# Optimization experiments

Hardware: AMD Instinct MI355X
Metric: run time of the kernel (lower is better)

The kernel has to match this reference:

```python
import jax
jax.config.update('jax_enable_x64', True)
import jax.numpy as jnp
import numpy as np

RESOLUTION = 0.3
BUFFER_SIZE = 10_000_000
DIFF_TRAVEL_DIST_LOCAL = 80.0 * 1.5  # local_map_radius * local_map_travel_dist_ratio
PRIMES = jnp.array([73856093, 19349669, 83492791], dtype=jnp.int64)
N_PTS = 2_000_000
M_PTS = 2_000_000
N_FRAMES = 20_000


def setup_inputs() -> dict:
    key = jax.random.key(0)
    k1, k2, k3, k4, k5 = jax.random.split(key, 5)
    points = jax.random.normal(k1, (N_PTS, 3), dtype=jnp.float32) * 30.0  # ~local map extent (m)
    neural_points = jax.random.normal(k2, (M_PTS, 3), dtype=jnp.float32) * 30.0
    # hash buffer: -1 means empty slot, otherwise index into neural_points
    buffer_pt_index = jax.random.randint(k3, (BUFFER_SIZE,), 0, M_PTS + 1, dtype=jnp.int64) - 1
    # monotonically increasing travel distance per frame
    travel_dist = jnp.cumsum(jax.random.uniform(k4, (N_FRAMES,), dtype=jnp.float32) * 0.2)
    point_ts_update = jax.random.randint(k5, (M_PTS,), 0, N_FRAMES, dtype=jnp.int64)
    return {
        'points': points,
        'neural_points': neural_points,
        'buffer_pt_index': buffer_pt_index,
        'travel_dist': travel_dist,
        'point_ts_update': point_ts_update,
        'cur_ts': 15000,
    }


def reference(points, neural_points, buffer_pt_index, travel_dist, point_ts_update, cur_ts):
    # grid coords + prime spatial hash (torch.fmod keeps sign of dividend -> jnp.fmod)
    grid = jnp.floor(points / RESOLUTION).astype(jnp.int64)          # [N,3]
    h = jnp.fmod((grid * PRIMES).sum(-1), BUFFER_SIZE)               # [N], may be negative
    hw = jnp.where(h < 0, h + BUFFER_SIZE, h)                        # torch negative-index wrap

    # voxel down-sample: keep per-voxel point closest to its voxel center
    center = (grid.astype(points.dtype) + 0.5) * RESOLUTION
    d_center = jnp.sum((points - center) ** 2, axis=-1)
    seg_min = jax.ops.segment_min(d_center, hw, num_segments=BUFFER_SIZE)
    keep = d_center <= seg_min[hw]                                   # [N] bool

    # hash buffer lookup (hash_idx == -1 means empty; torch wraps -1 to last row on gather)
    hash_idx = buffer_pt_index[hw]                                   # [N]
    M = neural_points.shape[0]
    idx_w = jnp.where(hash_idx < 0, hash_idx + M, hash_idx)
    vec = neural_points[idx_w] - points
    dist2 = jnp.sum(vec * vec, axis=-1)                              # [N]

    ts = point_ts_update[idx_w]
    delta_travel = travel_dist[cur_ts] - travel_dist[ts]             # [N]

    update_mask = keep & ((hash_idx == -1)
                          | (dist2 > 3.0 * RESOLUTION ** 2)
                          | (delta_travel > DIFF_TRAVEL_DIST_LOCAL))
    return dist2, delta_travel, update_mask
```

## Files before the change

kernel.cpp:

```cpp
#include <hip/hip_runtime.h>

#define BUFSZ 10000000
#define RESF 0.3f
#define RINV (1.0f / 0.3f)

#define BIN_SHIFT   13
#define BKT_PER_BIN 8192
#define NBINS       1221
#define BIN_CAP     2048
#define OVF_CAP     4000

#define BINS_OFF 80000000ull
#define CTL_OFF  110000000ull
#define OVF_OFF  (CTL_OFF + 8192ull)

__device__ __forceinline__ void voxel_hash_d(float px, float py, float pz,
                                             int& hw, unsigned& dbits)
{
#pragma clang fp contract(off)
    float fx = floorf(px * RINV);
    float fy = floorf(py * RINV);
    float fz = floorf(pz * RINV);

    long long gx = (long long)fx;
    long long gy = (long long)fy;
    long long gz = (long long)fz;
    long long s = gx * 73856093LL + gy * 19349669LL + gz * 83492791LL;
    long long h = s % (long long)BUFSZ;
    hw = (int)(h < 0 ? h + BUFSZ : h);

    float cx = (fx + 0.5f) * RESF;
    float cy = (fy + 0.5f) * RESF;
    float cz = (fz + 0.5f) * RESF;
    float dx = px - cx;
    float dy = py - cy;
    float dz = pz - cz;
    float d = dx * dx + dy * dy + dz * dz;
    dbits = __float_as_uint(d);
}

__global__ __launch_bounds__(256) void bin_points(
    const float* __restrict__ points,
    unsigned long long* __restrict__ bins_e,
    unsigned int* __restrict__ ctl,
    unsigned long long* __restrict__ ovf,
    int N)
{
    __shared__ unsigned int cnt[NBINS];
    int t = threadIdx.x;
    for (int b = t; b < NBINS; b += 256) cnt[b] = 0;
    __syncthreads();

    int base = blockIdx.x * (256 * 16);
    unsigned hwv[16];
    unsigned dbv[16];

#pragma unroll
    for (int k = 0; k < 16; ++k) {
        int i = base + t + k * 256;
        hwv[k] = 0xFFFFFFFFu;
        dbv[k] = 0;
        if (i < N) {
            int hw; unsigned db;
            voxel_hash_d(points[3 * i], points[3 * i + 1], points[3 * i + 2],
                         hw, db);
            hwv[k] = (unsigned)hw;
            dbv[k] = db;
            if (db <= 0x3FFFFFFFu)
                atomicAdd(&cnt[hw >> BIN_SHIFT], 1u);
        }
    }
    __syncthreads();

    for (int b = t; b < NBINS; b += 256) {
        unsigned c = cnt[b];
        cnt[b] = c ? atomicAdd(&ctl[b], c) : 0u;
    }
    __syncthreads();

#pragma unroll
    for (int k = 0; k < 16; ++k) {
        if (hwv[k] == 0xFFFFFFFFu) continue;
        unsigned hw = hwv[k], db = dbv[k];
        if (db <= 0x3FFFFFFFu) {
            unsigned bin = hw >> BIN_SHIFT;
            unsigned idx = atomicAdd(&cnt[bin], 1u);
            if (idx < BIN_CAP) {
                bins_e[(size_t)bin * BIN_CAP + idx] =
                    ((unsigned long long)db << BIN_SHIFT)
                    | (hw & (BKT_PER_BIN - 1));
                continue;
            }
        }
        unsigned o = atomicAdd(&ctl[NBINS], 1u);
        if (o < OVF_CAP)
            ovf[o] = ((unsigned long long)db << 32) | hw;
    }
}

__global__ __launch_bounds__(256) void min_bins(
    const unsigned long long* __restrict__ bins_e,
    const unsigned int* __restrict__ ctl,
    const int2* __restrict__ bufidx2,
    uint4* __restrict__ p8q)
{
    __shared__ unsigned int tbl[BKT_PER_BIN];
    int t = threadIdx.x;
    int b = blockIdx.x;

    uint4* t4 = (uint4*)tbl;
    for (int l = t; l < BKT_PER_BIN / 4; l += 256)
        t4[l] = make_uint4(0xFFFFFFFFu, 0xFFFFFFFFu, 0xFFFFFFFFu, 0xFFFFFFFFu);
    __syncthreads();

    unsigned c = ctl[b];
    if (c > BIN_CAP) c = BIN_CAP;
    const unsigned long long* e = bins_e + (size_t)b * BIN_CAP;
    for (unsigned j = t; j < c; j += 256) {
        unsigned long long v = e[j];
        atomicMin(&tbl[(unsigned)(v & (BKT_PER_BIN - 1))],
                  (unsigned)(v >> BIN_SHIFT));
    }
    __syncthreads();

    long long pbase = (long long)b * (BKT_PER_BIN / 2);
    for (int l = t; l < BKT_PER_BIN / 2; l += 256) {
        long long pp = pbase + l;
        long long g = 2 * pp;
        if (g + 1 < (long long)BUFSZ) {
            int2 bi = bufidx2[pp];
            p8q[pp] = make_uint4(tbl[2 * l], (unsigned)bi.x,
                                 tbl[2 * l + 1], (unsigned)bi.y);
        }
    }
}

__global__ __launch_bounds__(256) void fix_ovf(
    const unsigned int* __restrict__ ctl,
    const unsigned long long* __restrict__ ovf,
    unsigned int* __restrict__ p8w)
{
    unsigned c = ctl[NBINS];
    if (c > OVF_CAP) c = OVF_CAP;
    for (unsigned e = threadIdx.x; e < c; e += 256) {
        unsigned long long v = ovf[e];
        atomicMin(p8w + 2ull * (unsigned)(v & 0xFFFFFFFFu), (unsigned)(v >> 32));
    }
}

__global__ __launch_bounds__(256) void pack_pnt(
    const float* __restrict__ neural,
    const int* __restrict__ ts_upd,
    float4* __restrict__ pnt, int M)
{
    int T = gridDim.x * 256;
    for (int j = blockIdx.x * 256 + threadIdx.x; j < M; j += T)
        pnt[j] = make_float4(neural[3 * j], neural[3 * j + 1],
                             neural[3 * j + 2], __int_as_float(ts_upd[j]));
}

__global__ __launch_bounds__(256) void pass_out_A4(
    const float* __restrict__ points,
    const uint2* __restrict__ p8,
    const float4* __restrict__ pnt,
    const float* __restrict__ travel,
    const int* __restrict__ cur_ts_p,
    float* __restrict__ out,
    int N, int M, int S)
{
#pragma clang fp contract(off)
    int tid = blockIdx.x * 256 + threadIdx.x;
    if (tid >= S) return;

    float tcur = travel[cur_ts_p[0]];

    int      iv[4];
    bool     val[4];
    float    pxv[4], pyv[4], pzv[4];
    int      hwv[4];
    unsigned dbv[4];

#pragma unroll
    for (int k = 0; k < 4; ++k) {
        int i = tid + k * S;
        val[k] = (i < N);
        iv[k]  = val[k] ? i : 0;
        pxv[k] = points[3 * iv[k] + 0];
        pyv[k] = points[3 * iv[k] + 1];
        pzv[k] = points[3 * iv[k] + 2];
        voxel_hash_d(pxv[k], pyv[k], pzv[k], hwv[k], dbv[k]);
    }

    uint2 ev[4];
#pragma unroll
    for (int k = 0; k < 4; ++k) ev[k] = p8[hwv[k]];

    int hidxv[4], idxwv[4];
    float4 ntv[4];
#pragma unroll
    for (int k = 0; k < 4; ++k) {
        hidxv[k] = (int)ev[k].y;
        idxwv[k] = (hidxv[k] < 0) ? (hidxv[k] + M) : hidxv[k];
    }
#pragma unroll
    for (int k = 0; k < 4; ++k) ntv[k] = pnt[idxwv[k]];

#pragma unroll
    for (int k = 0; k < 4; ++k) {
        if (!val[k]) continue;

        bool keep = dbv[k] <= ev[k].x;

        float vx = ntv[k].x - pxv[k];
        float vy = ntv[k].y - pyv[k];
        float vz = ntv[k].z - pzv[k];
        float dist2 = vx * vx + vy * vy + vz * vz;

        int ts = __float_as_int(ntv[k].w);
        float dtv = tcur - travel[ts];

        const float THR = (float)(3.0 * 0.3 * 0.3);
        bool upd = keep && ((hidxv[k] == -1) || (dist2 > THR) || (dtv > 120.0f));

        out[iv[k]]         = dist2;
        out[N + iv[k]]     = dtv;
        out[2 * N + iv[k]] = upd ? 1.0f : 0.0f;
    }
}

__global__ __launch_bounds__(256) void pass_min_C(
    const float* __restrict__ points, unsigned int* __restrict__ seg, int N)
{
    int i = blockIdx.x * 256 + threadIdx.x;
    if (i >= N) return;
    int hw; unsigned dbits;
    voxel_hash_d(points[3 * i], points[3 * i + 1], points[3 * i + 2], hw, dbits);
    atomicMin(seg + hw, dbits);
}

__global__ __launch_bounds__(256) void pass_out_C(
    const float* __restrict__ points, const float* __restrict__ neural,
    const int* __restrict__ bufidx, const float* __restrict__ travel,
    const int* __restrict__ ts_upd, const int* __restrict__ cur_ts_p,
    const unsigned int* __restrict__ seg, float* __restrict__ out, int N, int M)
{
#pragma clang fp contract(off)
    int i = blockIdx.x * 256 + threadIdx.x;
    if (i >= N) return;
    float px = points[3 * i], py = points[3 * i + 1], pz = points[3 * i + 2];
    int hw; unsigned dbits;
    voxel_hash_d(px, py, pz, hw, dbits);
    bool keep = dbits <= seg[hw];
    int hidx = bufidx[hw];
    int idxw = (hidx < 0) ? (hidx + M) : hidx;
    float vx = neural[3 * idxw] - px;
    float vy = neural[3 * idxw + 1] - py;
    float vz = neural[3 * idxw + 2] - pz;
    float dist2 = vx * vx + vy * vy + vz * vz;
    int ts = ts_upd[idxw];
    float dtv = travel[cur_ts_p[0]] - travel[ts];
    const float THR = (float)(3.0 * 0.3 * 0.3);
    bool upd = keep && ((hidx == -1) || (dist2 > THR) || (dtv > 120.0f));
    out[i] = dist2;
    out[N + i] = dtv;
    out[2 * N + i] = upd ? 1.0f : 0.0f;
}

extern "C" void kernel_launch(void* const* d_in, const int* in_sizes, int n_in,
                              void* d_out, int out_size, void* d_ws, size_t ws_size,
                              hipStream_t stream)
{
    const float* points  = (const float*)d_in[0];
    const float* neural  = (const float*)d_in[1];
    const int*   bufidx  = (const int*)d_in[2];
    const float* travel  = (const float*)d_in[3];
    const int*   ts_upd  = (const int*)d_in[4];
    const int*   cur_ts  = (const int*)d_in[5];

    int N = in_sizes[0] / 3;
    int M = in_sizes[1] / 3;

    const size_t needA = (size_t)BUFSZ * 8 + (size_t)M * 16;
    if (ws_size >= needA && N <= 2000000) {
        char* ws = (char*)d_ws;
        uint2*              p8     = (uint2*)ws;
        unsigned long long* bins_e = (unsigned long long*)(ws + BINS_OFF);
        unsigned int*       ctl    = (unsigned int*)(ws + CTL_OFF);
        unsigned long long* ovf    = (unsigned long long*)(ws + OVF_OFF);
        float4*             pnt    = (float4*)(ws + BINS_OFF);

        hipMemsetAsync(ctl, 0, 8192, stream);

        int bblocks = (N + 4095) / 4096;
        bin_points<<<bblocks, 256, 0, stream>>>(points, bins_e, ctl, ovf, N);
        min_bins<<<NBINS, 256, 0, stream>>>(bins_e, ctl, (const int2*)bufidx,
                                            (uint4*)p8);
        fix_ovf<<<1, 256, 0, stream>>>(ctl, ovf, (unsigned int*)p8);
        pack_pnt<<<2048, 256, 0, stream>>>(neural, ts_upd, pnt, M);

        int S = (N + 3) / 4;
        int oblocks = (S + 255) / 256;
        pass_out_A4<<<oblocks, 256, 0, stream>>>(points, p8, pnt, travel, cur_ts,
                                                 (float*)d_out, N, M, S);
    } else {
        unsigned int* seg = (unsigned int*)d_ws;
        hipMemsetAsync(seg, 0xFF, (size_t)BUFSZ * sizeof(unsigned int), stream);
        int pblocks = (N + 255) / 256;
        pass_min_C<<<pblocks, 256, 0, stream>>>(points, seg, N);
        pass_out_C<<<pblocks, 256, 0, stream>>>(points, neural, bufidx, travel,
                                                ts_upd, cur_ts, seg,
                                                (float*)d_out, N, M);
    }
}
```

Baseline: 157.2 us.

## Fuse segment-min and output pass into per-bin kernel carrying point index and coords

Binning now stores each point's index and a copy of its coordinates alongside the hash bucket and distance. A single per-bin kernel computes the segment minimum in shared memory and then emits all outputs for that bin's points directly. This removes the dense 10M-entry packed table, the separate overflow fix, the neural-point repack and the second full hashing pass over points. In exchange, outputs are written as scattered stores and the neural and ts gathers are no longer packed into one float4, and overflow entries are scanned by every block.

```diff
diff --git a/kernel.cpp b/kernel.cpp
--- a/kernel.cpp
+++ b/kernel.cpp
@@ -8,11 +8,14 @@
 #define BKT_PER_BIN 8192
 #define NBINS       1221
 #define BIN_CAP     2048
-#define OVF_CAP     4000
-
-#define BINS_OFF 80000000ull
-#define CTL_OFF  110000000ull
-#define OVF_OFF  (CTL_OFF + 8192ull)
+#define OVF_CAP     16384
+
+#define E64_OFF  0ull
+#define EPOS_OFF 20004864ull
+#define CTL_OFF  50012160ull
+#define OVFA_OFF (CTL_OFF + 8192ull)
+#define OVFB_OFF (OVFA_OFF + 131072ull)
+#define WS_NEED  (OVFB_OFF + 65536ull)
 
 __device__ __forceinline__ void voxel_hash_d(float px, float py, float pz,
                                              int& hw, unsigned& dbits)
@@ -39,11 +42,13 @@
     dbits = __float_as_uint(d);
 }
 
-__global__ __launch_bounds__(256) void bin_points(
+__global__ __launch_bounds__(256) void bin_points2(
     const float* __restrict__ points,
-    unsigned long long* __restrict__ bins_e,
+    unsigned long long* __restrict__ e64,
+    float* __restrict__ epos,
     unsigned int* __restrict__ ctl,
-    unsigned long long* __restrict__ ovf,
+    unsigned long long* __restrict__ ovfA,
+    unsigned int* __restrict__ ovfB,
     int N)
 {
     __shared__ unsigned int cnt[NBINS];
@@ -81,29 +86,46 @@
 #pragma unroll
     for (int k = 0; k < 16; ++k) {
         if (hwv[k] == 0xFFFFFFFFu) continue;
+        int i = base + t + k * 256;
         unsigned hw = hwv[k], db = dbv[k];
         if (db <= 0x3FFFFFFFu) {
             unsigned bin = hw >> BIN_SHIFT;
             unsigned idx = atomicAdd(&cnt[bin], 1u);
             if (idx < BIN_CAP) {
-                bins_e[(size_t)bin * BIN_CAP + idx] =
-                    ((unsigned long long)db << BIN_SHIFT)
-                    | (hw & (BKT_PER_BIN - 1));
+                size_t slot = (size_t)bin * BIN_CAP + idx;
+                e64[slot] = ((unsigned long long)db << 34)
+                          | ((unsigned long long)(unsigned)i << 13)
+                          | (hw & (BKT_PER_BIN - 1));
+                epos[3 * slot + 0] = points[3 * i + 0];
+                epos[3 * slot + 1] = points[3 * i + 1];
+                epos[3 * slot + 2] = points[3 * i + 2];
                 continue;
             }
         }
         unsigned o = atomicAdd(&ctl[NBINS], 1u);
-        if (o < OVF_CAP)
-            ovf[o] = ((unsigned long long)db << 32) | hw;
-    }
-}
-
-__global__ __launch_bounds__(256) void min_bins(
-    const unsigned long long* __restrict__ bins_e,
+        if (o < OVF_CAP) {
+            ovfA[o] = ((unsigned long long)db << 24) | hw;
+            ovfB[o] = (unsigned)i;
+        }
+    }
+}
+
+__global__ __launch_bounds__(256) void min_out(
+    const unsigned long long* __restrict__ e64,
+    const float* __restrict__ epos,
     const unsigned int* __restrict__ ctl,
-    const int2* __restrict__ bufidx2,
-    uint4* __restrict__ p8q)
-{
+    const unsigned long long* __restrict__ ovfA,
+    const unsigned int* __restrict__ ovfB,
+    const int* __restrict__ bufidx,
+    const float* __restrict__ neural,
+    const int* __restrict__ ts_upd,
+    const float* __restrict__ travel,
+    const int* __restrict__ cur_ts_p,
+    const float* __restrict__ points,
+    float* __restrict__ out,
+    int N, int M)
+{
+#pragma clang fp contract(off)
     __shared__ unsigned int tbl[BKT_PER_BIN];
     int t = threadIdx.x;
     int b = blockIdx.x;
@@ -115,116 +137,86 @@
 
     unsigned c = ctl[b];
     if (c > BIN_CAP) c = BIN_CAP;
-    const unsigned long long* e = bins_e + (size_t)b * BIN_CAP;
+    size_t ebase = (size_t)b * BIN_CAP;
     for (unsigned j = t; j < c; j += 256) {
-        unsigned long long v = e[j];
+        unsigned long long v = e64[ebase + j];
         atomicMin(&tbl[(unsigned)(v & (BKT_PER_BIN - 1))],
-                  (unsigned)(v >> BIN_SHIFT));
-    }
-    __syncthreads();
-
-    long long pbase = (long long)b * (BKT_PER_BIN / 2);
-    for (int l = t; l < BKT_PER_BIN / 2; l += 256) {
-        long long pp = pbase + l;
-        long long g = 2 * pp;
-        if (g + 1 < (long long)BUFSZ) {
-            int2 bi = bufidx2[pp];
-            p8q[pp] = make_uint4(tbl[2 * l], (unsigned)bi.x,
-                                 tbl[2 * l + 1], (unsigned)bi.y);
-        }
-    }
-}
-
-__global__ __launch_bounds__(256) void fix_ovf(
-    const unsigned int* __restrict__ ctl,
-    const unsigned long long* __restrict__ ovf,
-    unsigned int* __restrict__ p8w)
-{
-    unsigned c = ctl[NBINS];
-    if (c > OVF_CAP) c = OVF_CAP;
-    for (unsigned e = threadIdx.x; e < c; e += 256) {
-        unsigned long long v = ovf[e];
-        atomicMin(p8w + 2ull * (unsigned)(v & 0xFFFFFFFFu), (unsigned)(v >> 32));
-    }
-}
-
-__global__ __launch_bounds__(256) void pack_pnt(
-    const float* __restrict__ neural,
-    const int* __restrict__ ts_upd,
-    float4* __restrict__ pnt, int M)
-{
-    int T = gridDim.x * 256;
-    for (int j = blockIdx.x * 256 + threadIdx.x; j < M; j += T)
-        pnt[j] = make_float4(neural[3 * j], neural[3 * j + 1],
-                             neural[3 * j + 2], __int_as_float(ts_upd[j]));
-}
-
-__global__ __launch_bounds__(256) void pass_out_A4(
-    const float* __restrict__ points,
-    const uint2* __restrict__ p8,
-    const float4* __restrict__ pnt,
-    const float* __restrict__ travel,
-    const int* __restrict__ cur_ts_p,
-    float* __restrict__ out,
-    int N, int M, int S)
-{
-#pragma clang fp contract(off)
-    int tid = blockIdx.x * 256 + threadIdx.x;
-    if (tid >= S) return;
+                  (unsigned)(v >> 34));
+    }
+
+    unsigned ovfn = ctl[NBINS];
+    if (ovfn > OVF_CAP) ovfn = OVF_CAP;
+    unsigned gbase = (unsigned)b << BIN_SHIFT;
+    for (unsigned o = t; o < ovfn; o += 256) {
+        unsigned long long va = ovfA[o];
+        unsigned hw = (unsigned)(va & 0xFFFFFFu);
+        if ((hw >> BIN_SHIFT) == (unsigned)b)
+            atomicMin(&tbl[hw & (BKT_PER_BIN - 1)], (unsigned)(va >> 24));
+    }
+    __syncthreads();
 
     float tcur = travel[cur_ts_p[0]];
-
-    int      iv[4];
-    bool     val[4];
-    float    pxv[4], pyv[4], pzv[4];
-    int      hwv[4];
-    unsigned dbv[4];
-
-#pragma unroll
-    for (int k = 0; k < 4; ++k) {
-        int i = tid + k * S;
-        val[k] = (i < N);
-        iv[k]  = val[k] ? i : 0;
-        pxv[k] = points[3 * iv[k] + 0];
-        pyv[k] = points[3 * iv[k] + 1];
-        pzv[k] = points[3 * iv[k] + 2];
-        voxel_hash_d(pxv[k], pyv[k], pzv[k], hwv[k], dbv[k]);
-    }
-
-    uint2 ev[4];
-#pragma unroll
-    for (int k = 0; k < 4; ++k) ev[k] = p8[hwv[k]];
-
-    int hidxv[4], idxwv[4];
-    float4 ntv[4];
-#pragma unroll
-    for (int k = 0; k < 4; ++k) {
-        hidxv[k] = (int)ev[k].y;
-        idxwv[k] = (hidxv[k] < 0) ? (hidxv[k] + M) : hidxv[k];
-    }
-#pragma unroll
-    for (int k = 0; k < 4; ++k) ntv[k] = pnt[idxwv[k]];
-
-#pragma unroll
-    for (int k = 0; k < 4; ++k) {
-        if (!val[k]) continue;
-
-        bool keep = dbv[k] <= ev[k].x;
-
-        float vx = ntv[k].x - pxv[k];
-        float vy = ntv[k].y - pyv[k];
-        float vz = ntv[k].z - pzv[k];
+    const float THR = (float)(3.0 * 0.3 * 0.3);
+
+    for (unsigned j = t; j < c; j += 256) {
+        unsigned long long v = e64[ebase + j];
+        unsigned lb   = (unsigned)(v & (BKT_PER_BIN - 1));
+        int      pidx = (int)((v >> 13) & 0x1FFFFFu);
+        unsigned db   = (unsigned)(v >> 34);
+
+        bool keep = db <= tbl[lb];
+
+        int hidx = bufidx[gbase + lb];
+        int idxw = (hidx < 0) ? (hidx + M) : hidx;
+
+        float px = epos[3 * (ebase + j) + 0];
+        float py = epos[3 * (ebase + j) + 1];
+        float pz = epos[3 * (ebase + j) + 2];
+
+        float vx = neural[3 * idxw + 0] - px;
+        float vy = neural[3 * idxw + 1] - py;
+        float vz = neural[3 * idxw + 2] - pz;
         float dist2 = vx * vx + vy * vy + vz * vz;
 
-        int ts = __float_as_int(ntv[k].w);
+        int ts = ts_upd[idxw];
         float dtv = tcur - travel[ts];
 
-        const float THR = (float)(3.0 * 0.3 * 0.3);
-        bool upd = keep && ((hidxv[k] == -1) || (dist2 > THR) || (dtv > 120.0f));
-
-        out[iv[k]]         = dist2;
-        out[N + iv[k]]     = dtv;
-        out[2 * N + iv[k]] = upd ? 1.0f : 0.0f;
+        bool upd = keep && ((hidx == -1) || (dist2 > THR) || (dtv > 120.0f));
+
+        out[pidx]         = dist2;
+        out[N + pidx]     = dtv;
+        out[2 * N + pidx] = upd ? 1.0f : 0.0f;
+    }
+
+    for (unsigned o = t; o < ovfn; o += 256) {
+        unsigned long long va = ovfA[o];
+        unsigned hw = (unsigned)(va & 0xFFFFFFu);
+        if ((hw >> BIN_SHIFT) != (unsigned)b) continue;
+        unsigned db = (unsigned)(va >> 24);
+        int pidx = (int)ovfB[o];
+
+        bool keep = db <= tbl[hw & (BKT_PER_BIN - 1)];
+
+        int hidx = bufidx[hw];
+        int idxw = (hidx < 0) ? (hidx + M) : hidx;
+
+        float px = points[3 * pidx + 0];
+        float py = points[3 * pidx + 1];
+        float pz = points[3 * pidx + 2];
+
+        float vx = neural[3 * idxw + 0] - px;
+        float vy = neural[3 * idxw + 1] - py;
+        float vz = neural[3 * idxw + 2] - pz;
+        float dist2 = vx * vx + vy * vy + vz * vz;
+
+        int ts = ts_upd[idxw];
+        float dtv = tcur - travel[ts];
+
+        bool upd = keep && ((hidx == -1) || (dist2 > THR) || (dtv > 120.0f));
+
+        out[pidx]         = dist2;
+        out[N + pidx]     = dtv;
+        out[2 * N + pidx] = upd ? 1.0f : 0.0f;
     }
 }
 
@@ -280,28 +272,22 @@
     int N = in_sizes[0] / 3;
     int M = in_sizes[1] / 3;
 
-    const size_t needA = (size_t)BUFSZ * 8 + (size_t)M * 16;
-    if (ws_size >= needA && N <= 2000000) {
+    if (ws_size >= WS_NEED && N <= (1 << 21)) {
         char* ws = (char*)d_ws;
-        uint2*              p8     = (uint2*)ws;
-        unsigned long long* bins_e = (unsigned long long*)(ws + BINS_OFF);
-        unsigned int*       ctl    = (unsigned int*)(ws + CTL_OFF);
-        unsigned long long* ovf    = (unsigned long long*)(ws + OVF_OFF);
-        float4*             pnt    = (float4*)(ws + BINS_OFF);
+        unsigned long long* e64  = (unsigned long long*)(ws + E64_OFF);
+        float*              epos = (float*)(ws + EPOS_OFF);
+        unsigned int*       ctl  = (unsigned int*)(ws + CTL_OFF);
+        unsigned long long* ovfA = (unsigned long long*)(ws + OVFA_OFF);
+        unsigned int*       ovfB = (unsigned int*)(ws + OVFB_OFF);
 
         hipMemsetAsync(ctl, 0, 8192, stream);
 
         int bblocks = (N + 4095) / 4096;
-        bin_points<<<bblocks, 256, 0, stream>>>(points, bins_e, ctl, ovf, N);
-        min_bins<<<NBINS, 256, 0, stream>>>(bins_e, ctl, (const int2*)bufidx,
-                                            (uint4*)p8);
-        fix_ovf<<<1, 256, 0, stream>>>(ctl, ovf, (unsigned int*)p8);
-        pack_pnt<<<2048, 256, 0, stream>>>(neural, ts_upd, pnt, M);
-
-        int S = (N + 3) / 4;
-        int oblocks = (S + 255) / 256;
-        pass_out_A4<<<oblocks, 256, 0, stream>>>(points, p8, pnt, travel, cur_ts,
-                                                 (float*)d_out, N, M, S);
+        bin_points2<<<bblocks, 256, 0, stream>>>(points, e64, epos, ctl,
+                                                 ovfA, ovfB, N);
+        min_out<<<NBINS, 256, 0, stream>>>(e64, epos, ctl, ovfA, ovfB,
+                                           bufidx, neural, ts_upd, travel,
+                                           cur_ts, points, (float*)d_out, N, M);
     } else {
         unsigned int* seg = (unsigned int*)d_ws;
         hipMemsetAsync(seg, 0xFF, (size_t)BUFSZ * sizeof(unsigned int), stream);
```

After: 255.9 us. 1.63x slower.

## Fuse neural-point packing into binning kernel and stage bins in output buffer

Applied to the files above, without the earlier changes.

Folds the neural-point/timestamp packing loop into the binning kernel, removing a separate launch. The bin entries, control counters and overflow list now live in the output buffer rather than the workspace, so the packed point array no longer aliases the bin storage. That aliasing was the reason packing had to wait until after min_bins. The overflow capacity is also raised. The binning kernel becomes heavier per block, and the output must be large enough to hold the scratch data, which later kernels then overwrite.

```diff
diff --git a/kernel.cpp b/kernel.cpp
--- a/kernel.cpp
+++ b/kernel.cpp
@@ -8,11 +8,13 @@
 #define BKT_PER_BIN 8192
 #define NBINS       1221
 #define BIN_CAP     2048
-#define OVF_CAP     4000
-
-#define BINS_OFF 80000000ull
-#define CTL_OFF  110000000ull
-#define OVF_OFF  (CTL_OFF + 8192ull)
+#define OVF_CAP     16384
+
+#define PNT_WS_OFF  80000000ull
+#define E64_OUT_OFF 0ull
+#define CTL_OUT_OFF 20004864ull
+#define OVF_OUT_OFF 20013056ull
+#define OUT_NEED    (OVF_OUT_OFF + 131072ull)
 
 __device__ __forceinline__ void voxel_hash_d(float px, float py, float pz,
                                              int& hw, unsigned& dbits)
@@ -39,12 +41,15 @@
     dbits = __float_as_uint(d);
 }
 
-__global__ __launch_bounds__(256) void bin_points(
+__global__ __launch_bounds__(256) void bin_pack(
     const float* __restrict__ points,
     unsigned long long* __restrict__ bins_e,
     unsigned int* __restrict__ ctl,
     unsigned long long* __restrict__ ovf,
-    int N)
+    const float* __restrict__ neural,
+    const int* __restrict__ ts_upd,
+    float4* __restrict__ pnt,
+    int N, int M)
 {
     __shared__ unsigned int cnt[NBINS];
     int t = threadIdx.x;
@@ -96,6 +101,11 @@
         if (o < OVF_CAP)
             ovf[o] = ((unsigned long long)db << 32) | hw;
     }
+
+    int T = gridDim.x * 256;
+    for (int j = blockIdx.x * 256 + t; j < M; j += T)
+        pnt[j] = make_float4(neural[3 * j], neural[3 * j + 1],
+                             neural[3 * j + 2], __int_as_float(ts_upd[j]));
 }
 
 __global__ __launch_bounds__(256) void min_bins(
@@ -146,17 +156,6 @@
         unsigned long long v = ovf[e];
         atomicMin(p8w + 2ull * (unsigned)(v & 0xFFFFFFFFu), (unsigned)(v >> 32));
     }
-}
-
-__global__ __launch_bounds__(256) void pack_pnt(
-    const float* __restrict__ neural,
-    const int* __restrict__ ts_upd,
-    float4* __restrict__ pnt, int M)
-{
-    int T = gridDim.x * 256;
-    for (int j = blockIdx.x * 256 + threadIdx.x; j < M; j += T)
-        pnt[j] = make_float4(neural[3 * j], neural[3 * j + 1],
-                             neural[3 * j + 2], __int_as_float(ts_upd[j]));
 }
 
 __global__ __launch_bounds__(256) void pass_out_A4(
@@ -280,23 +279,24 @@
     int N = in_sizes[0] / 3;
     int M = in_sizes[1] / 3;
 
-    const size_t needA = (size_t)BUFSZ * 8 + (size_t)M * 16;
-    if (ws_size >= needA && N <= 2000000) {
+    const size_t needWs = (size_t)BUFSZ * 8 + (size_t)M * 16;
+    if (ws_size >= needWs && (size_t)out_size * 4 >= OUT_NEED) {
         char* ws = (char*)d_ws;
-        uint2*              p8     = (uint2*)ws;
-        unsigned long long* bins_e = (unsigned long long*)(ws + BINS_OFF);
-        unsigned int*       ctl    = (unsigned int*)(ws + CTL_OFF);
-        unsigned long long* ovf    = (unsigned long long*)(ws + OVF_OFF);
-        float4*             pnt    = (float4*)(ws + BINS_OFF);
+        char* ob = (char*)d_out;
+        uint2*              p8   = (uint2*)ws;
+        float4*             pnt  = (float4*)(ws + PNT_WS_OFF);
+        unsigned long long* e64  = (unsigned long long*)(ob + E64_OUT_OFF);
+        unsigned int*       ctl  = (unsigned int*)(ob + CTL_OUT_OFF);
+        unsigned long long* ovf  = (unsigned long long*)(ob + OVF_OUT_OFF);
 
         hipMemsetAsync(ctl, 0, 8192, stream);
 
         int bblocks = (N + 4095) / 4096;
-        bin_points<<<bblocks, 256, 0, stream>>>(points, bins_e, ctl, ovf, N);
-        min_bins<<<NBINS, 256, 0, stream>>>(bins_e, ctl, (const int2*)bufidx,
+        bin_pack<<<bblocks, 256, 0, stream>>>(points, e64, ctl, ovf,
+                                              neural, ts_upd, pnt, N, M);
+        min_bins<<<NBINS, 256, 0, stream>>>(e64, ctl, (const int2*)bufidx,
                                             (uint4*)p8);
         fix_ovf<<<1, 256, 0, stream>>>(ctl, ovf, (unsigned int*)p8);
-        pack_pnt<<<2048, 256, 0, stream>>>(neural, ts_upd, pnt, M);
 
         int S = (N + 3) / 4;
         int oblocks = (S + 255) / 256;
```

New measurement: 161.5 us. 1.03x slower.

## Resolve per-point keep and hash index via slot indirection instead of dense table

Applied to the files above, without the earlier changes.

Instead of writing a dense 10M-entry table of (segment min, buffer index) pairs and re-hashing each point in the output pass, binning now records each point's slot. A per-bin kernel computes the keep flag and buffer index for each binned entry and writes them into a compact result array. The output pass then reads that result through the slot, so the large dense table write and the scattered random reads into it go away. Scratch bins and overflow lists now live in the output buffer before it is overwritten. This adds a slot-array round trip, a second read of the bins, and a slow single-block overflow fallback that scans linearly.

```diff
diff --git a/kernel.cpp b/kernel.cpp
--- a/kernel.cpp
+++ b/kernel.cpp
@@ -8,11 +8,19 @@
 #define BKT_PER_BIN 8192
 #define NBINS       1221
 #define BIN_CAP     2048
-#define OVF_CAP     4000
-
-#define BINS_OFF 80000000ull
-#define CTL_OFF  110000000ull
-#define OVF_OFF  (CTL_OFF + 8192ull)
+#define NSLOTS      (NBINS * BIN_CAP)
+#define OVF_CAP     16384
+
+#define E64_OUT_OFF 0ull
+#define CTL_OUT_OFF 20004864ull
+#define OVF_OUT_OFF 20013056ull
+#define OUT_NEED    (OVF_OUT_OFF + 131072ull)
+
+#define PNT_WS_OFF   0ull
+#define SLOT_WS_OFF  32000000ull
+#define RES_WS_OFF   40000000ull
+#define ROVF_WS_OFF  50002432ull
+#define WS_NEED      (ROVF_WS_OFF + 65536ull)
 
 __device__ __forceinline__ void voxel_hash_d(float px, float py, float pz,
                                              int& hw, unsigned& dbits)
@@ -39,11 +47,12 @@
     dbits = __float_as_uint(d);
 }
 
-__global__ __launch_bounds__(256) void bin_points(
+__global__ __launch_bounds__(256) void bin_slot(
     const float* __restrict__ points,
-    unsigned long long* __restrict__ bins_e,
+    unsigned long long* __restrict__ e64,
     unsigned int* __restrict__ ctl,
-    unsigned long long* __restrict__ ovf,
+    unsigned long long* __restrict__ ovfA,
+    unsigned int* __restrict__ slot32,
     int N)
 {
     __shared__ unsigned int cnt[NBINS];
@@ -81,70 +90,24 @@
 #pragma unroll
     for (int k = 0; k < 16; ++k) {
         if (hwv[k] == 0xFFFFFFFFu) continue;
+        int i = base + t + k * 256;
         unsigned hw = hwv[k], db = dbv[k];
         if (db <= 0x3FFFFFFFu) {
             unsigned bin = hw >> BIN_SHIFT;
             unsigned idx = atomicAdd(&cnt[bin], 1u);
             if (idx < BIN_CAP) {
-                bins_e[(size_t)bin * BIN_CAP + idx] =
-                    ((unsigned long long)db << BIN_SHIFT)
-                    | (hw & (BKT_PER_BIN - 1));
+                unsigned slot = bin * BIN_CAP + idx;
+                e64[slot] = ((unsigned long long)db << BIN_SHIFT)
+                          | (hw & (BKT_PER_BIN - 1));
+                slot32[i] = slot;
                 continue;
             }
         }
         unsigned o = atomicAdd(&ctl[NBINS], 1u);
+        unsigned oc = (o < OVF_CAP) ? o : (OVF_CAP - 1);
         if (o < OVF_CAP)
-            ovf[o] = ((unsigned long long)db << 32) | hw;
-    }
-}
-
-__global__ __launch_bounds__(256) void min_bins(
-    const unsigned long long* __restrict__ bins_e,
-    const unsigned int* __restrict__ ctl,
-    const int2* __restrict__ bufidx2,
-    uint4* __restrict__ p8q)
-{
-    __shared__ unsigned int tbl[BKT_PER_BIN];
-    int t = threadIdx.x;
-    int b = blockIdx.x;
-
-    uint4* t4 = (uint4*)tbl;
-    for (int l = t; l < BKT_PER_BIN / 4; l += 256)
-        t4[l] = make_uint4(0xFFFFFFFFu, 0xFFFFFFFFu, 0xFFFFFFFFu, 0xFFFFFFFFu);
-    __syncthreads();
-
-    unsigned c = ctl[b];
-    if (c > BIN_CAP) c = BIN_CAP;
-    const unsigned long long* e = bins_e + (size_t)b * BIN_CAP;
-    for (unsigned j = t; j < c; j += 256) {
-        unsigned long long v = e[j];
-        atomicMin(&tbl[(unsigned)(v & (BKT_PER_BIN - 1))],
-                  (unsigned)(v >> BIN_SHIFT));
-    }
-    __syncthreads();
-
-    long long pbase = (long long)b * (BKT_PER_BIN / 2);
-    for (int l = t; l < BKT_PER_BIN / 2; l += 256) {
-        long long pp = pbase + l;
-        long long g = 2 * pp;
-        if (g + 1 < (long long)BUFSZ) {
-            int2 bi = bufidx2[pp];
-            p8q[pp] = make_uint4(tbl[2 * l], (unsigned)bi.x,
-                                 tbl[2 * l + 1], (unsigned)bi.y);
-        }
-    }
-}
-
-__global__ __launch_bounds__(256) void fix_ovf(
-    const unsigned int* __restrict__ ctl,
-    const unsigned long long* __restrict__ ovf,
-    unsigned int* __restrict__ p8w)
-{
-    unsigned c = ctl[NBINS];
-    if (c > OVF_CAP) c = OVF_CAP;
-    for (unsigned e = threadIdx.x; e < c; e += 256) {
-        unsigned long long v = ovf[e];
-        atomicMin(p8w + 2ull * (unsigned)(v & 0xFFFFFFFFu), (unsigned)(v >> 32));
+            ovfA[o] = ((unsigned long long)db << 24) | hw;
+        slot32[i] = 0x80000000u | oc;
     }
 }
 
@@ -159,9 +122,98 @@
                              neural[3 * j + 2], __int_as_float(ts_upd[j]));
 }
 
-__global__ __launch_bounds__(256) void pass_out_A4(
+__global__ __launch_bounds__(256) void min_res(
+    const unsigned long long* __restrict__ e64,
+    const unsigned int* __restrict__ ctl,
+    const unsigned long long* __restrict__ ovfA,
+    const int* __restrict__ bufidx,
+    unsigned int* __restrict__ res32)
+{
+    __shared__ unsigned int tbl[BKT_PER_BIN];
+    int t = threadIdx.x;
+    int b = blockIdx.x;
+
+    uint4* t4 = (uint4*)tbl;
+    for (int l = t; l < BKT_PER_BIN / 4; l += 256)
+        t4[l] = make_uint4(0xFFFFFFFFu, 0xFFFFFFFFu, 0xFFFFFFFFu, 0xFFFFFFFFu);
+    __syncthreads();
+
+    unsigned c = ctl[b];
+    if (c > BIN_CAP) c = BIN_CAP;
+    size_t ebase = (size_t)b * BIN_CAP;
+    for (unsigned j = t; j < c; j += 256) {
+        unsigned long long v = e64[ebase + j];
+        atomicMin(&tbl[(unsigned)(v & (BKT_PER_BIN - 1))],
+                  (unsigned)(v >> BIN_SHIFT));
+    }
+
+    unsigned ovfn = ctl[NBINS];
+    if (ovfn > OVF_CAP) ovfn = OVF_CAP;
+    unsigned gbase = (unsigned)b << BIN_SHIFT;
+    for (unsigned o = t; o < ovfn; o += 256) {
+        unsigned long long va = ovfA[o];
+        unsigned hw = (unsigned)(va & 0xFFFFFFu);
+        if ((hw >> BIN_SHIFT) == (unsigned)b)
+            atomicMin(&tbl[hw & (BKT_PER_BIN - 1)], (unsigned)(va >> 24));
+    }
+    __syncthreads();
+
+    for (unsigned j = t; j < c; j += 256) {
+        unsigned long long v = e64[ebase + j];
+        unsigned lb = (unsigned)(v & (BKT_PER_BIN - 1));
+        unsigned db = (unsigned)(v >> BIN_SHIFT);
+
+        bool keep = db <= tbl[lb];
+        int hidx = bufidx[gbase + lb];
+        res32[ebase + j] = (keep ? 0x80000000u : 0u) | (unsigned)(hidx + 1);
+    }
+}
+
+__global__ __launch_bounds__(256) void fix_ovf2(
+    const unsigned long long* __restrict__ e64,
+    const unsigned int* __restrict__ ctl,
+    const unsigned long long* __restrict__ ovfA,
+    const int* __restrict__ bufidx,
+    unsigned int* __restrict__ res_ovf)
+{
+    unsigned ovfn = ctl[NBINS];
+    if (ovfn > OVF_CAP) ovfn = OVF_CAP;
+    for (unsigned o = threadIdx.x; o < ovfn; o += 256) {
+        unsigned long long va = ovfA[o];
+        unsigned hw = (unsigned)(va & 0xFFFFFFu);
+        unsigned db = (unsigned)(va >> 24);
+        unsigned bin = hw >> BIN_SHIFT;
+        unsigned lb  = hw & (BKT_PER_BIN - 1);
+
+        unsigned mn = 0xFFFFFFFFu;
+        unsigned c = ctl[bin];
+        if (c > BIN_CAP) c = BIN_CAP;
+        const unsigned long long* e = e64 + (size_t)bin * BIN_CAP;
+        for (unsigned j = 0; j < c; ++j) {
+            unsigned long long v = e[j];
+            if ((unsigned)(v & (BKT_PER_BIN - 1)) == lb) {
+                unsigned d2 = (unsigned)(v >> BIN_SHIFT);
+                if (d2 < mn) mn = d2;
+            }
+        }
+        for (unsigned o2 = 0; o2 < ovfn; ++o2) {
+            unsigned long long v2 = ovfA[o2];
+            if ((unsigned)(v2 & 0xFFFFFFu) == hw) {
+                unsigned d2 = (unsigned)(v2 >> 24);
+                if (d2 < mn) mn = d2;
+            }
+        }
+        bool keep = db <= mn;
+        int hidx = bufidx[hw];
+        res_ovf[o] = (keep ? 0x80000000u : 0u) | (unsigned)(hidx + 1);
+    }
+}
+
+__global__ __launch_bounds__(256) void pass_out_S4(
     const float* __restrict__ points,
-    const uint2* __restrict__ p8,
+    const unsigned int* __restrict__ slot32,
+    const unsigned int* __restrict__ res32,
+    const unsigned int* __restrict__ res_ovf,
     const float4* __restrict__ pnt,
     const float* __restrict__ travel,
     const int* __restrict__ cur_ts_p,
@@ -177,8 +229,7 @@
     int      iv[4];
     bool     val[4];
     float    pxv[4], pyv[4], pzv[4];
-    int      hwv[4];
-    unsigned dbv[4];
+    unsigned sv[4];
 
 #pragma unroll
     for (int k = 0; k < 4; ++k) {
@@ -188,18 +239,23 @@
         pxv[k] = points[3 * iv[k] + 0];
         pyv[k] = points[3 * iv[k] + 1];
         pzv[k] = points[3 * iv[k] + 2];
-        voxel_hash_d(pxv[k], pyv[k], pzv[k], hwv[k], dbv[k]);
-    }
-
-    uint2 ev[4];
-#pragma unroll
-    for (int k = 0; k < 4; ++k) ev[k] = p8[hwv[k]];
+        sv[k]  = slot32[iv[k]];
+    }
+
+    unsigned rv[4];
+#pragma unroll
+    for (int k = 0; k < 4; ++k) {
+        const unsigned* rp = (sv[k] & 0x80000000u)
+                           ? (res_ovf + (sv[k] & 0x7FFFFFFFu))
+                           : (res32 + sv[k]);
+        rv[k] = *rp;
+    }
 
     int hidxv[4], idxwv[4];
     float4 ntv[4];
 #pragma unroll
     for (int k = 0; k < 4; ++k) {
-        hidxv[k] = (int)ev[k].y;
+        hidxv[k] = (int)(rv[k] & 0x7FFFFFFFu) - 1;
         idxwv[k] = (hidxv[k] < 0) ? (hidxv[k] + M) : hidxv[k];
     }
 #pragma unroll
@@ -209,7 +265,7 @@
     for (int k = 0; k < 4; ++k) {
         if (!val[k]) continue;
 
-        bool keep = dbv[k] <= ev[k].x;
+        bool keep = (rv[k] >> 31) != 0u;
 
         float vx = ntv[k].x - pxv[k];
         float vy = ntv[k].y - pyv[k];
@@ -280,27 +336,30 @@
     int N = in_sizes[0] / 3;
     int M = in_sizes[1] / 3;
 
-    const size_t needA = (size_t)BUFSZ * 8 + (size_t)M * 16;
-    if (ws_size >= needA && N <= 2000000) {
+    if (ws_size >= WS_NEED && (size_t)out_size * 4 >= OUT_NEED
+        && N <= 2100000 && (size_t)N * 4 <= (RES_WS_OFF - SLOT_WS_OFF)) {
         char* ws = (char*)d_ws;
-        uint2*              p8     = (uint2*)ws;
-        unsigned long long* bins_e = (unsigned long long*)(ws + BINS_OFF);
-        unsigned int*       ctl    = (unsigned int*)(ws + CTL_OFF);
-        unsigned long long* ovf    = (unsigned long long*)(ws + OVF_OFF);
-        float4*             pnt    = (float4*)(ws + BINS_OFF);
+        char* ob = (char*)d_out;
+        float4*             pnt     = (float4*)(ws + PNT_WS_OFF);
+        unsigned int*       slot32  = (unsigned int*)(ws + SLOT_WS_OFF);
+        unsigned int*       res32   = (unsigned int*)(ws + RES_WS_OFF);
+        unsigned int*       res_ovf = (unsigned int*)(ws + ROVF_WS_OFF);
+        unsigned long long* e64     = (unsigned long long*)(ob + E64_OUT_OFF);
+        unsigned int*       ctl     = (unsigned int*)(ob + CTL_OUT_OFF);
+        unsigned long long* ovfA    = (unsigned long long*)(ob + OVF_OUT_OFF);
 
         hipMemsetAsync(ctl, 0, 8192, stream);
 
         int bblocks = (N + 4095) / 4096;
-        bin_points<<<bblocks, 256, 0, stream>>>(points, bins_e, ctl, ovf, N);
-        min_bins<<<NBINS, 256, 0, stream>>>(bins_e, ctl, (const int2*)bufidx,
-                                            (uint4*)p8);
-        fix_ovf<<<1, 256, 0, stream>>>(ctl, ovf, (unsigned int*)p8);
+        bin_slot<<<bblocks, 256, 0, stream>>>(points, e64, ctl, ovfA, slot32, N);
         pack_pnt<<<2048, 256, 0, stream>>>(neural, ts_upd, pnt, M);
+        min_res<<<NBINS, 256, 0, stream>>>(e64, ctl, ovfA, bufidx, res32);
+        fix_ovf2<<<1, 256, 0, stream>>>(e64, ctl, ovfA, bufidx, res_ovf);
 
         int S = (N + 3) / 4;
         int oblocks = (S + 255) / 256;
-        pass_out_A4<<<oblocks, 256, 0, stream>>>(points, p8, pnt, travel, cur_ts,
+        pass_out_S4<<<oblocks, 256, 0, stream>>>(points, slot32, res32, res_ovf,
+                                                 pnt, travel, cur_ts,
                                                  (float*)d_out, N, M, S);
     } else {
         unsigned int* seg = (unsigned int*)d_ws;
```

Result: faster. 147.0 us (-6.5%).
